# Kernel optimization log

Hardware: AMD Instinct MI355X
Metric: run time of the kernel (lower is better)

The kernel has to match this reference:

```python
import jax, jax.numpy as jnp
import numpy as np

B, C, H, W = 256, 3, 128, 128
K = 16                      # vae_small.img_size == kernel == stride (non-overlapping)
GH, GW = H // K, W // K
P = C * K * K               # 768 flattened patch dim
HID = 2048
L = 256                     # latent_size


def setup_inputs() -> dict:
    key = jax.random.key(0)
    ks = jax.random.split(key, 9)
    s = 0.02
    f32 = jnp.float32
    return {
        "x": jax.random.uniform(ks[0], (B, C, H, W), f32),
        "w_enc1": jax.random.normal(ks[1], (P, HID), f32) * s,
        "b_enc1": jnp.zeros((HID,), f32),
        "w_enc2": jax.random.normal(ks[2], (HID, 2 * L), f32) * s,
        "b_enc2": jnp.zeros((2 * L,), f32),
        "w_dec1": jax.random.normal(ks[3], (L, HID), f32) * s,
        "b_dec1": jnp.zeros((HID,), f32),
        "w_dec2": jax.random.normal(ks[4], (HID, P), f32) * s,
        "b_dec2": jnp.zeros((P,), f32),
    }


def reference(x, w_enc1, b_enc1, w_enc2, b_enc2, w_dec1, b_dec1, w_dec2, b_dec2):
    b, c, h, w = x.shape
    gh, gw = h // K, w // K
    # unfold: [b,c,h,w] -> [b,gh,gw, c*K*K]  (same padding is 0 when stride==k)
    patches = (x.reshape(b, c, gh, K, gw, K)
                .transpose(0, 2, 4, 1, 3, 5)
                .reshape(b, gh, gw, c * K * K))
    # batched per-patch VAE encode (replaces the python map/unbind loop)
    he = jax.nn.relu(patches @ w_enc1 + b_enc1)            # [b,gh,gw,HID]
    mu_logvar = he @ w_enc2 + b_enc2                        # [b,gh,gw,2L]
    mu = mu_logvar[..., :L]
    z = mu                                                  # deterministic reparameterize
    # batched per-patch decode
    hd = jax.nn.relu(z @ w_dec1 + b_dec1)                   # [b,gh,gw,HID]
    dec = jax.nn.sigmoid(hd @ w_dec2 + b_dec2)              # [b,gh,gw,P]
    # fold: exact inverse of unfold since stride == kernel
    recon_x = (dec.reshape(b, gh, gw, c, K, K)
                 .transpose(0, 3, 1, 4, 2, 5)
                 .reshape(b, c, h, w))
    mu_logvar_2d = jnp.transpose(mu_logvar, (0, 3, 1, 2))   # [b, 2L, gh, gw]
    return recon_x, mu_logvar_2d
```

## Files before the change

kernel.cpp:

```cpp
#include <hip/hip_runtime.h>
#include <hip/hip_bf16.h>
#include <stdint.h>

typedef __bf16 bf16x8_t __attribute__((ext_vector_type(8)));
typedef float f32x4_t __attribute__((ext_vector_type(4)));
typedef unsigned short ushort8_t __attribute__((ext_vector_type(8)));

__device__ __forceinline__ unsigned short f2bf(float f) {
    union { float f; uint32_t i; } v; v.f = f;
    uint32_t i = v.i + (((v.i >> 16) & 1u) + 0x7FFFu);
    return (unsigned short)(i >> 16);
}

typedef const __attribute__((address_space(1))) void* gas_t;
typedef __attribute__((address_space(3))) void* las_t;
__device__ __forceinline__ void load_lds16(const unsigned short* g, unsigned short* l) {
    __builtin_amdgcn_global_load_lds((gas_t)g, (las_t)l, 16, 0, 0);
}

#define BB   256
#define CC   3
#define HH   128
#define WW   128
#define PP   768
#define HID  2048
#define LL   256
#define MM   16384

__global__ void patchify(const float* __restrict__ x,
                         unsigned short* __restrict__ patches) {
    int t = blockIdx.x * 256 + threadIdx.x;
    int e = t * 8;
    int col = e & 127;
    int row = (e >> 7) & 127;
    int c   = (e >> 14) % 3;
    int b   = e / (128 * 128 * 3);
    int gh = row >> 4, kh = row & 15, gw = col >> 4, kw = col & 15;
    long po = (long)(b * 64 + gh * 8 + gw) * PP + c * 256 + kh * 16 + kw;
    float4 v0 = *(const float4*)(x + e);
    float4 v1 = *(const float4*)(x + e + 4);
    ushort8_t o;
    o[0] = f2bf(v0.x); o[1] = f2bf(v0.y); o[2] = f2bf(v0.z); o[3] = f2bf(v0.w);
    o[4] = f2bf(v1.x); o[5] = f2bf(v1.y); o[6] = f2bf(v1.z); o[7] = f2bf(v1.w);
    *(ushort8_t*)(patches + po) = o;
}

__global__ void transpose_k(const float* __restrict__ in,
                            unsigned short* __restrict__ out, int R, int C) {
    __shared__ unsigned short tile[32][34];
    int nbc = C >> 5;
    int tc = blockIdx.x % nbc, tr = blockIdx.x / nbc;
    int tx = threadIdx.x & 31, ty0 = threadIdx.x >> 5;
    int r0 = tr << 5, c0 = tc << 5;
    #pragma unroll
    for (int i = 0; i < 4; ++i) {
        int ty = ty0 + i * 8;
        tile[ty][tx] = f2bf(in[(long)(r0 + ty) * C + c0 + tx]);
    }
    __syncthreads();
    #pragma unroll
    for (int i = 0; i < 4; ++i) {
        int ty = ty0 + i * 8;
        out[(long)(c0 + ty) * R + r0 + tx] = tile[tx][ty];
    }
}

template <int ACT, int WMODE>
__global__ void __launch_bounds__(256)
gemm_bt(const unsigned short* __restrict__ A, int lda,
        const unsigned short* __restrict__ Bt,
        const float* __restrict__ bias,
        unsigned short* __restrict__ C0u,
        float* __restrict__ C0f,
        float* __restrict__ C1f,
        int ldc, int Kd, int nbn, int m0) {
    __shared__ __align__(16) unsigned short As[128 * 64];
    __shared__ __align__(16) unsigned short Bs[128 * 64];
    const int nbm = gridDim.x / nbn;
    const int stripe = nbm >> 3;
    const int xcd = blockIdx.x & 7;
    const int loc = blockIdx.x >> 3;
    const int bm = xcd * stripe + (loc % stripe);
    const int bn = loc / stripe;
    const int tid = threadIdx.x;
    const int wave = tid >> 6;
    const int lane = tid & 63;
    const int wm = (wave >> 1) << 6;
    const int wn = (wave & 1) << 6;
    const int srow = (wave << 3) + (lane >> 3);
    const int scol = (((lane & 7) ^ (lane >> 3)) << 3);
    const unsigned short* Ab = A + (long)(bm * 128) * lda;
    const unsigned short* Bb = Bt + (long)(bn * 128) * Kd;

    f32x4_t acc[4][4];
    #pragma unroll
    for (int i = 0; i < 4; ++i)
        #pragma unroll
        for (int j = 0; j < 4; ++j)
            acc[i][j] = (f32x4_t){0.f, 0.f, 0.f, 0.f};

    const int fr = lane & 15;
    const int quad = lane >> 4;

    for (int k0 = 0; k0 < Kd; k0 += 64) {
        #pragma unroll
        for (int i = 0; i < 4; ++i) {
            load_lds16(Ab + (long)(srow + i * 32) * lda + k0 + scol,
                       As + ((i * 32 + (wave << 3)) << 6));
            load_lds16(Bb + (long)(srow + i * 32) * Kd + k0 + scol,
                       Bs + ((i * 32 + (wave << 3)) << 6));
        }
        __syncthreads();
        #pragma unroll
        for (int h = 0; h < 2; ++h) {
            bf16x8_t af[4], bfr[4];
            #pragma unroll
            for (int i = 0; i < 4; ++i) {
                const int row = wm + (i << 4) + fr;
                const int pg = (quad + (h << 2)) ^ (fr & 7);
                af[i] = *(const bf16x8_t*)&As[(row << 6) + (pg << 3)];
            }
            #pragma unroll
            for (int j = 0; j < 4; ++j) {
                const int row = wn + (j << 4) + fr;
                const int pg = (quad + (h << 2)) ^ (fr & 7);
                bfr[j] = *(const bf16x8_t*)&Bs[(row << 6) + (pg << 3)];
            }
            #pragma unroll
            for (int i = 0; i < 4; ++i)
                #pragma unroll
                for (int j = 0; j < 4; ++j)
                    acc[i][j] = __builtin_amdgcn_mfma_f32_16x16x32_bf16(
                        af[i], bfr[j], acc[i][j], 0, 0, 0);
        }
        __syncthreads();
    }

    const int gcol0 = bn * 128 + wn;
    const int grow0 = bm * 128 + wm;
    #pragma unroll
    for (int j = 0; j < 4; ++j) {
        const int n = gcol0 + (j << 4) + (lane & 15);
        const float bv = bias[n];
        #pragma unroll
        for (int i = 0; i < 4; ++i) {
            #pragma unroll
            for (int r = 0; r < 4; ++r) {
                const int m = grow0 + (i << 4) + ((lane >> 4) << 2) + r;
                float v = acc[i][j][r] + bv;
                if (ACT == 1) v = fmaxf(v, 0.f);
                if (ACT == 2) v = 1.f / (1.f + __expf(-v));
                if (WMODE == 0) {
                    C0u[(long)m * ldc + n] = f2bf(v);
                } else if (WMODE == 1) {
                    const int gm = m0 + m;
                    C1f[((long)(gm >> 6) * 512 + n) * 64 + (gm & 63)] = v;
                    if (n < 256) C0u[(long)m * 256 + n] = f2bf(v);
                } else {
                    const int gm = m0 + m;
                    const int b = gm >> 6, g6 = gm & 63;
                    const int gh = g6 >> 3, gw = g6 & 7;
                    const int c = n >> 8, kh = (n >> 4) & 15, kw = n & 15;
                    const long o = (long)(b * 3 + c) * 16384
                                 + ((gh << 4) + kh) * 128 + (gw << 4) + kw;
                    C0f[o] = v;
                }
            }
        }
    }
}

extern "C" void kernel_launch(void* const* d_in, const int* in_sizes, int n_in,
                              void* d_out, int out_size, void* d_ws, size_t ws_size,
                              hipStream_t stream) {
    const float* x      = (const float*)d_in[0];
    const float* w_enc1 = (const float*)d_in[1];
    const float* b_enc1 = (const float*)d_in[2];
    const float* w_enc2 = (const float*)d_in[3];
    const float* b_enc2 = (const float*)d_in[4];
    const float* w_dec1 = (const float*)d_in[5];
    const float* b_dec1 = (const float*)d_in[6];
    const float* w_dec2 = (const float*)d_in[7];
    const float* b_dec2 = (const float*)d_in[8];
    float* outf = (float*)d_out;
    unsigned short* patches = (unsigned short*)d_out;
    float* out_ml = outf + (long)MM * PP;

    const size_t WT_ELEMS = 2048 * 768 + 512 * 2048 + 2048 * 256 + 768 * 2048;
    unsigned short* sb;
    long Mc;
    if (ws_size >= (WT_ELEMS + (size_t)MM * (LL + HID)) * 2) {
        sb = (unsigned short*)d_ws;  Mc = MM;
    } else {
        sb = (unsigned short*)d_in[0]; Mc = 8192;
    }
    unsigned short* wT1 = sb;
    unsigned short* wT2 = wT1 + 2048 * 768;
    unsigned short* wT3 = wT2 + 512 * 2048;
    unsigned short* wT4 = wT3 + 2048 * 256;
    unsigned short* mu  = wT4 + 768 * 2048;
    unsigned short* he  = mu + Mc * LL;

    patchify<<<6144, 256, 0, stream>>>(x, patches);

    transpose_k<<<(768 / 32) * (2048 / 32), 256, 0, stream>>>(w_enc1, wT1, 768, 2048);
    transpose_k<<<(2048 / 32) * (512 / 32), 256, 0, stream>>>(w_enc2, wT2, 2048, 512);
    transpose_k<<<(256 / 32) * (2048 / 32), 256, 0, stream>>>(w_dec1, wT3, 256, 2048);
    transpose_k<<<(2048 / 32) * (768 / 32), 256, 0, stream>>>(w_dec2, wT4, 2048, 768);

    const int nbm = (int)(Mc / 128);
    for (long m0 = MM - Mc; m0 >= 0; m0 -= Mc) {
        gemm_bt<1, 0><<<nbm * (HID / 128), 256, 0, stream>>>(
            patches + m0 * PP, PP, wT1, b_enc1,
            he, nullptr, nullptr, HID, PP, HID / 128, 0);
        gemm_bt<0, 1><<<nbm * (512 / 128), 256, 0, stream>>>(
            he, HID, wT2, b_enc2,
            mu, nullptr, out_ml, 0, HID, 512 / 128, (int)m0);
        gemm_bt<1, 0><<<nbm * (HID / 128), 256, 0, stream>>>(
            mu, LL, wT3, b_dec1,
            he, nullptr, nullptr, HID, LL, HID / 128, 0);
        gemm_bt<2, 2><<<nbm * (PP / 128), 256, 0, stream>>>(
            he, HID, wT4, b_dec2,
            nullptr, outf, nullptr, 0, HID, PP / 128, (int)m0);
    }
}
```

Before: 383.5 us.

## Use 256x256 GEMM tiles with 512 threads and double-buffered LDS

Each GEMM block now computes a 256x256 output tile with 8 waves instead of 128x128 with 4. The K step shrinks from 64 to 32, and the LDS is double-buffered so the next tile's global-to-LDS load is issued before computing the current one, which needs only one barrier per iteration. The aim is more operand reuse per byte loaded and hiding load latency. The cost is 32 accumulators per thread, which raises register pressure, and fewer blocks per grid: for example, 16384/256 * 2 = 128 blocks for the 512-wide encoder GEMM. The swizzle also changes to a new row-dependent rotation.

```diff
diff --git a/kernel.cpp b/kernel.cpp
--- a/kernel.cpp
+++ b/kernel.cpp
@@ -66,7 +66,7 @@
 }
 
 template <int ACT, int WMODE>
-__global__ void __launch_bounds__(256)
+__global__ void __launch_bounds__(512, 2)
 gemm_bt(const unsigned short* __restrict__ A, int lda,
         const unsigned short* __restrict__ Bt,
         const float* __restrict__ bias,
@@ -74,8 +74,8 @@
         float* __restrict__ C0f,
         float* __restrict__ C1f,
         int ldc, int Kd, int nbn, int m0) {
-    __shared__ __align__(16) unsigned short As[128 * 64];
-    __shared__ __align__(16) unsigned short Bs[128 * 64];
+    __shared__ __align__(16) unsigned short As[2][256 * 32];
+    __shared__ __align__(16) unsigned short Bs[2][256 * 32];
     const int nbm = gridDim.x / nbn;
     const int stripe = nbm >> 3;
     const int xcd = blockIdx.x & 7;
@@ -86,67 +86,77 @@
     const int wave = tid >> 6;
     const int lane = tid & 63;
     const int wm = (wave >> 1) << 6;
-    const int wn = (wave & 1) << 6;
-    const int srow = (wave << 3) + (lane >> 3);
-    const int scol = (((lane & 7) ^ (lane >> 3)) << 3);
-    const unsigned short* Ab = A + (long)(bm * 128) * lda;
-    const unsigned short* Bb = Bt + (long)(bn * 128) * Kd;
-
-    f32x4_t acc[4][4];
+    const int wn = (wave & 1) << 7;
+    const int srow = (wave << 4) + (lane >> 2);
+    const int spg  = lane & 3;
+    const unsigned short* Ab = A + (long)(bm * 256) * lda;
+    const unsigned short* Bb = Bt + (long)(bn * 256) * Kd;
+
+    f32x4_t acc[4][8];
     #pragma unroll
     for (int i = 0; i < 4; ++i)
         #pragma unroll
-        for (int j = 0; j < 4; ++j)
+        for (int j = 0; j < 8; ++j)
             acc[i][j] = (f32x4_t){0.f, 0.f, 0.f, 0.f};
 
     const int fr = lane & 15;
     const int quad = lane >> 4;
 
-    for (int k0 = 0; k0 < Kd; k0 += 64) {
+#define STAGE(p, k0)                                                         \
+    {                                                                        \
+        _Pragma("unroll")                                                    \
+        for (int i_ = 0; i_ < 2; ++i_) {                                     \
+            const int row_ = srow + (i_ << 7);                               \
+            const int g_ = ((spg - (row_ >> 1)) & 3) << 3;                   \
+            load_lds16(Ab + (long)row_ * lda + (k0) + g_,                    \
+                       &As[p][((i_ << 7) + (wave << 4)) << 5]);              \
+            load_lds16(Bb + (long)row_ * Kd + (k0) + g_,                     \
+                       &Bs[p][((i_ << 7) + (wave << 4)) << 5]);              \
+        }                                                                    \
+    }
+
+    const int iters = Kd >> 5;
+    STAGE(0, 0);
+    __syncthreads();
+    for (int it = 0; it < iters; ++it) {
+        const int p = it & 1;
+        if (it + 1 < iters) STAGE(p ^ 1, (it + 1) << 5);
+        const unsigned short* Ap = As[p];
+        const unsigned short* Bp = Bs[p];
+        bf16x8_t af[4], bfr[8];
         #pragma unroll
         for (int i = 0; i < 4; ++i) {
-            load_lds16(Ab + (long)(srow + i * 32) * lda + k0 + scol,
-                       As + ((i * 32 + (wave << 3)) << 6));
-            load_lds16(Bb + (long)(srow + i * 32) * Kd + k0 + scol,
-                       Bs + ((i * 32 + (wave << 3)) << 6));
+            const int row = wm + (i << 4) + fr;
+            const int pg = ((quad + (row >> 1)) & 3) << 3;
+            af[i] = *(const bf16x8_t*)&Ap[(row << 5) + pg];
         }
+        #pragma unroll
+        for (int j = 0; j < 8; ++j) {
+            const int row = wn + (j << 4) + fr;
+            const int pg = ((quad + (row >> 1)) & 3) << 3;
+            bfr[j] = *(const bf16x8_t*)&Bp[(row << 5) + pg];
+        }
+        #pragma unroll
+        for (int i = 0; i < 4; ++i)
+            #pragma unroll
+            for (int j = 0; j < 8; ++j)
+                acc[i][j] = __builtin_amdgcn_mfma_f32_16x16x32_bf16(
+                    af[i], bfr[j], acc[i][j], 0, 0, 0);
         __syncthreads();
-        #pragma unroll
-        for (int h = 0; h < 2; ++h) {
-            bf16x8_t af[4], bfr[4];
-            #pragma unroll
-            for (int i = 0; i < 4; ++i) {
-                const int row = wm + (i << 4) + fr;
-                const int pg = (quad + (h << 2)) ^ (fr & 7);
-                af[i] = *(const bf16x8_t*)&As[(row << 6) + (pg << 3)];
-            }
-            #pragma unroll
-            for (int j = 0; j < 4; ++j) {
-                const int row = wn + (j << 4) + fr;
-                const int pg = (quad + (h << 2)) ^ (fr & 7);
-                bfr[j] = *(const bf16x8_t*)&Bs[(row << 6) + (pg << 3)];
-            }
-            #pragma unroll
-            for (int i = 0; i < 4; ++i)
-                #pragma unroll
-                for (int j = 0; j < 4; ++j)
-                    acc[i][j] = __builtin_amdgcn_mfma_f32_16x16x32_bf16(
-                        af[i], bfr[j], acc[i][j], 0, 0, 0);
-        }
-        __syncthreads();
-    }
-
-    const int gcol0 = bn * 128 + wn;
-    const int grow0 = bm * 128 + wm;
-    #pragma unroll
-    for (int j = 0; j < 4; ++j) {
-        const int n = gcol0 + (j << 4) + (lane & 15);
+    }
+#undef STAGE
+
+    const int gcol0 = bn * 256 + wn;
+    const int grow0 = bm * 256 + wm;
+    #pragma unroll
+    for (int j = 0; j < 8; ++j) {
+        const int n = gcol0 + (j << 4) + fr;
         const float bv = bias[n];
         #pragma unroll
         for (int i = 0; i < 4; ++i) {
             #pragma unroll
             for (int r = 0; r < 4; ++r) {
-                const int m = grow0 + (i << 4) + ((lane >> 4) << 2) + r;
+                const int m = grow0 + (i << 4) + (quad << 2) + r;
                 float v = acc[i][j][r] + bv;
                 if (ACT == 1) v = fmaxf(v, 0.f);
                 if (ACT == 2) v = 1.f / (1.f + __expf(-v));
@@ -208,19 +218,19 @@
     transpose_k<<<(256 / 32) * (2048 / 32), 256, 0, stream>>>(w_dec1, wT3, 256, 2048);
     transpose_k<<<(2048 / 32) * (768 / 32), 256, 0, stream>>>(w_dec2, wT4, 2048, 768);
 
-    const int nbm = (int)(Mc / 128);
+    const int nbm = (int)(Mc / 256);
     for (long m0 = MM - Mc; m0 >= 0; m0 -= Mc) {
-        gemm_bt<1, 0><<<nbm * (HID / 128), 256, 0, stream>>>(
+        gemm_bt<1, 0><<<nbm * (HID / 256), 512, 0, stream>>>(
             patches + m0 * PP, PP, wT1, b_enc1,
-            he, nullptr, nullptr, HID, PP, HID / 128, 0);
-        gemm_bt<0, 1><<<nbm * (512 / 128), 256, 0, stream>>>(
+            he, nullptr, nullptr, HID, PP, HID / 256, 0);
+        gemm_bt<0, 1><<<nbm * (512 / 256), 512, 0, stream>>>(
             he, HID, wT2, b_enc2,
-            mu, nullptr, out_ml, 0, HID, 512 / 128, (int)m0);
-        gemm_bt<1, 0><<<nbm * (HID / 128), 256, 0, stream>>>(
+            mu, nullptr, out_ml, 0, HID, 512 / 256, (int)m0);
+        gemm_bt<1, 0><<<nbm * (HID / 256), 512, 0, stream>>>(
             mu, LL, wT3, b_dec1,
-            he, nullptr, nullptr, HID, LL, HID / 128, 0);
-        gemm_bt<2, 2><<<nbm * (PP / 128), 256, 0, stream>>>(
+            he, nullptr, nullptr, HID, LL, HID / 256, 0);
+        gemm_bt<2, 2><<<nbm * (PP / 256), 512, 0, stream>>>(
             he, HID, wT4, b_dec2,
-            nullptr, outf, nullptr, 0, HID, PP / 128, (int)m0);
-    }
-}
+            nullptr, outf, nullptr, 0, HID, PP / 256, (int)m0);
+    }
+}
```

Measured after the change: 422.9 us. 1.1x slower.
